# Kernel tuning notes

Hardware: AMD Instinct MI355X
Metric: run time of the kernel (lower is better)

The kernel has to match this reference:

```python
import jax, jax.numpy as jnp
import numpy as np

N_NODES = 32768
N_EDGES = 524288
NODE_DIM = 128
HIDDEN = 256
EDGE_DIM = 32


def setup_inputs() -> dict:
    key = jax.random.key(0)
    ks = jax.random.split(key, 12)
    s = 0.05
    return {
        "h": jax.random.normal(ks[0], (N_NODES, NODE_DIM), jnp.float32),
        "x": jax.random.normal(ks[1], (N_NODES, 3), jnp.float32) * 10.0,
        "edge_index": jax.random.randint(ks[2], (2, N_EDGES), 0, N_NODES, dtype=jnp.int32).astype(jnp.int64),
        "edge_dist": jax.random.uniform(ks[3], (N_EDGES,), jnp.float32) * 15.0,
        # edge_mlp: Linear(1, edge_dim) -> SiLU -> Linear(edge_dim, edge_dim)
        "We1": jax.random.normal(ks[4], (1, EDGE_DIM), jnp.float32) * s,
        "be1": jnp.zeros((EDGE_DIM,), jnp.float32),
        "We2": jax.random.normal(ks[5], (EDGE_DIM, EDGE_DIM), jnp.float32) * s,
        "be2": jnp.zeros((EDGE_DIM,), jnp.float32),
        # node_mlp: Linear(2*node+edge, hidden) -> SiLU -> Linear(hidden, node)
        "Wn1": jax.random.normal(ks[6], (2 * NODE_DIM + EDGE_DIM, HIDDEN), jnp.float32) * s,
        "bn1": jnp.zeros((HIDDEN,), jnp.float32),
        "Wn2": jax.random.normal(ks[7], (HIDDEN, NODE_DIM), jnp.float32) * s,
        "bn2": jnp.zeros((NODE_DIM,), jnp.float32),
        # coord_mlp: Linear(2*node+edge, hidden) -> SiLU -> Linear(hidden, 1, bias=False)
        "Wc1": jax.random.normal(ks[8], (2 * NODE_DIM + EDGE_DIM, HIDDEN), jnp.float32) * s,
        "bc1": jnp.zeros((HIDDEN,), jnp.float32),
        "Wc2": jax.random.normal(ks[9], (HIDDEN, 1), jnp.float32) * s,
    }


def reference(h, x, edge_index, edge_dist,
              We1, be1, We2, be2,
              Wn1, bn1, Wn2, bn2,
              Wc1, bc1, Wc2):
    src, dst = edge_index[0], edge_index[1]
    n_nodes = h.shape[0]

    # edge_mlp on scalar distances -> [E, edge_dim]
    edge_attr = jax.nn.silu(edge_dist[:, None] @ We1 + be1) @ We2 + be2

    # per-edge message input: [E, 2*node_dim + edge_dim]
    m_input = jnp.concatenate([h[src], h[dst], edge_attr], axis=-1)

    # node messages and scatter-add onto destination nodes
    m = jax.nn.silu(m_input @ Wn1 + bn1) @ Wn2 + bn2          # [E, node_dim]
    h_agg = jax.ops.segment_sum(m, dst, num_segments=n_nodes)  # [N, node_dim]

    # equivariant coordinate update along normalized edge direction
    coord_weight = jax.nn.silu(m_input @ Wc1 + bc1) @ Wc2      # [E, 1]
    dir_vec = x[src] - x[dst]                                  # [E, 3]
    dir_len = jnp.maximum(jnp.linalg.norm(dir_vec, axis=-1, keepdims=True), 1e-8)
    coord_update = coord_weight * (dir_vec / dir_len)          # [E, 3]
    x_agg = jax.ops.segment_sum(coord_update, dst, num_segments=n_nodes)

    return h + h_agg, x + x_agg
```

## Files before the change

kernel.cpp:

```cpp
#include <hip/hip_runtime.h>
#include <math.h>

#define N_NODES 32768
#define N_EDGES 524288
#define NODE_DIM 128
#define HIDDEN 256
#define EDGE_DIM 32
#define TE 64
#define NBLK (N_EDGES / TE)
#define ASTR 296
#define HSTR 264
#define MSTR 132

typedef __attribute__((ext_vector_type(8))) short bf16x8;
typedef __attribute__((ext_vector_type(16))) float f32x16;

__device__ __forceinline__ float silu_f(float v) {
    float e = __expf(-v);
    return v * __builtin_amdgcn_rcpf(1.0f + e);
}

__device__ __forceinline__ unsigned short f2bf_rne(float f) {
    union { float f; unsigned int u; } v; v.f = f;
    return (unsigned short)((v.u + 0x7fffu + ((v.u >> 16) & 1u)) >> 16);
}
__device__ __forceinline__ unsigned int pk_rne(float a, float b) {
    return (unsigned int)f2bf_rne(a) | ((unsigned int)f2bf_rne(b) << 16);
}
__device__ __forceinline__ unsigned int pkbf(float a, float b) {
    union { float f; unsigned int u; } ua, ub; ua.f = a; ub.f = b;
    return __builtin_amdgcn_perm(ub.u + 0x8000u, ua.u + 0x8000u, 0x07060302u);
}
__device__ __forceinline__ unsigned short f2bf_hu(float f) {
    union { float f; unsigned int u; } v; v.f = f;
    return (unsigned short)((v.u + 0x8000u) >> 16);
}

__device__ __forceinline__ int detect_is64(const void* ei, int t) {
    const unsigned int* ew = (const unsigned int*)ei;
    unsigned int hiw = ew[2 * (t & 63) + 1];
    return (__ballot(hiw != 0u) == 0ULL) ? 1 : 0;
}

#define WS_BIAS_OFF 1024
#define WS_W1S_OFF  69632
#define WS_W2S_OFF  364544
#define WS_CNT_OFF  430080
#define WS_CUR_OFF  561152
#define WS_PERM_OFF 692224
#define WS_PART_OFF 2789376
#define WS_HBF_OFF  2790400
#define WS_HBF_END  (WS_HBF_OFF + N_NODES * NODE_DIM * 2)

#define SEG_CNT  32768
#define SEG_W1S  147456
#define SEG_W2S  32768
#define SEG_BIAS 512
#define SEG_OUT  1073152
#define SEG_HBF  524288
#define PREP_TOT (SEG_CNT + SEG_W1S + SEG_W2S + SEG_BIAS + SEG_OUT + SEG_HBF)

__global__ void prep_all_kernel(const float* __restrict__ h, const float* __restrict__ x,
                                const float* __restrict__ We2, const float* __restrict__ be2,
                                const float* __restrict__ Wn1, const float* __restrict__ bn1,
                                const float* __restrict__ Wn2,
                                const float* __restrict__ Wc1, const float* __restrict__ bc1,
                                float* __restrict__ out, float* __restrict__ biasC,
                                unsigned short* __restrict__ W1s, unsigned short* __restrict__ W2s,
                                int* __restrict__ counts, unsigned short* __restrict__ hbf) {
    int i = blockIdx.x * 256 + threadIdx.x;
    if (i < SEG_CNT) { counts[i] = 0; return; }
    i -= SEG_CNT;
    if (i < SEG_W1S) {
        int jj = i & 7, ln = (i >> 3) & 63, rest = i >> 9;
        int step = rest % 18, tile = rest / 18;
        int n = tile * 32 + (ln & 31);
        int k = step * 16 + ((ln >> 5) * 8) + jj;
        float v;
        if (k < 256) {
            v = (n < 256) ? Wn1[k * 256 + n] : Wc1[k * 256 + (n - 256)];
        } else {
            int j = k - 256;
            float s = 0.0f;
            #pragma unroll 8
            for (int q = 0; q < 32; ++q)
                s += We2[j * 32 + q] * ((n < 256) ? Wn1[(256 + q) * 256 + n]
                                                  : Wc1[(256 + q) * 256 + (n - 256)]);
            v = s;
        }
        W1s[i] = f2bf_rne(v);
        return;
    }
    i -= SEG_W1S;
    if (i < SEG_W2S) {
        int jj = i & 7, ln = (i >> 3) & 63, rest = i >> 9;
        int step = rest & 15, tile = rest >> 4;
        int d = tile * 32 + (ln & 31);
        int k = step * 16 + ((ln >> 5) * 8) + jj;
        W2s[i] = f2bf_rne(Wn2[k * 128 + d]);
        return;
    }
    i -= SEG_W2S;
    if (i < SEG_BIAS) {
        int n = i;
        float s = (n < 256) ? bn1[n] : bc1[n - 256];
        #pragma unroll 8
        for (int q = 0; q < 32; ++q)
            s += be2[q] * ((n < 256) ? Wn1[(256 + q) * 256 + n]
                                     : Wc1[(256 + q) * 256 + (n - 256)]);
        biasC[n] = s;
        return;
    }
    i -= SEG_BIAS;
    if (i < SEG_OUT) {
        const int NH4 = N_NODES * NODE_DIM / 4;
        const float4* h4 = (const float4*)h;
        const float4* x4 = (const float4*)x;
        ((float4*)out)[i] = (i < NH4) ? h4[i] : x4[i - NH4];
        return;
    }
    i -= SEG_OUT;
    if (hbf != nullptr && i < SEG_HBF) {
        const float4* p = (const float4*)&h[i * 8];
        float4 v0 = p[0], v1 = p[1];
        uint4 o = make_uint4(pk_rne(v0.x, v0.y), pk_rne(v0.z, v0.w),
                             pk_rne(v1.x, v1.y), pk_rne(v1.z, v1.w));
        *(uint4*)&hbf[i * 8] = o;
    }
}

__global__ void hist_kernel(const void* __restrict__ ei, int* __restrict__ counts) {
    int is64 = detect_is64(ei, threadIdx.x);
    int e = blockIdx.x * 256 + threadIdx.x;
    int dst = is64 ? (int)((const long long*)ei)[N_EDGES + e]
                   : ((const int*)ei)[N_EDGES + e];
    atomicAdd(&counts[dst], 1);
}

__global__ __launch_bounds__(256)
void scanA_kernel(const int* __restrict__ counts, int* __restrict__ partials) {
    __shared__ int red[256];
    const int t = threadIdx.x;
    const int b = blockIdx.x;
    red[t] = counts[b * 256 + t];
    __syncthreads();
    #pragma unroll
    for (int s = 128; s > 0; s >>= 1) {
        if (t < s) red[t] += red[t + s];
        __syncthreads();
    }
    if (t == 0) partials[b] = red[0];
}

__global__ __launch_bounds__(256)
void scanC_kernel(const int* __restrict__ counts, const int* __restrict__ partials,
                  int* __restrict__ cursor) {
    __shared__ int pb[128];
    __shared__ int loc[256];
    const int t = threadIdx.x;
    const int b = blockIdx.x;
    if (t < 128) pb[t] = partials[t];
    int c = counts[b * 256 + t];
    loc[t] = c;
    __syncthreads();
    if (t == 0) {
        int s = 0;
        for (int j = 0; j < 128; ++j) { int v = pb[j]; pb[j] = s; s += v; }
    }
    #pragma unroll
    for (int d = 1; d < 256; d <<= 1) {
        int v = (t >= d) ? loc[t - d] : 0;
        __syncthreads();
        loc[t] += v;
        __syncthreads();
    }
    cursor[b * 256 + t] = pb[b] + loc[t] - c;
}

__global__ void place_kernel(const void* __restrict__ ei,
                             int* __restrict__ cursor, int* __restrict__ perm) {
    int is64 = detect_is64(ei, threadIdx.x);
    int e = blockIdx.x * 256 + threadIdx.x;
    int dst = is64 ? (int)((const long long*)ei)[N_EDGES + e]
                   : ((const int*)ei)[N_EDGES + e];
    int pos = atomicAdd(&cursor[dst], 1);
    perm[pos] = e;
}

__global__ __launch_bounds__(512, 4)
void egnn_mfma_kernel(const float* __restrict__ h, const float* __restrict__ x,
                      const void* __restrict__ ei, const float* __restrict__ dist,
                      const float* __restrict__ We1, const float* __restrict__ be1,
                      const float* __restrict__ bn2, const float* __restrict__ Wc2,
                      const float* __restrict__ biasC,
                      const unsigned short* __restrict__ W1s,
                      const unsigned short* __restrict__ W2s,
                      const int* __restrict__ perm,
                      const unsigned short* __restrict__ hbf,
                      float* __restrict__ out)
{
    __shared__ unsigned short smA[TE * ASTR];
    __shared__ int sidx[TE], didx[TE], eidx[TE];
    __shared__ float cw_s[TE];
    __shared__ float cxyz[3 * TE];

    unsigned short* smH = smA;
    float* smM = (float*)smA;

    const int t = threadIdx.x;
    const int lane = t & 63;
    const int wv = t >> 6;
    const int lo = lane & 31;
    const int hi = lane >> 5;
    const int swz = ((blockIdx.x & 7) * (NBLK / 8)) + (blockIdx.x >> 3);
    const int ebase = swz * TE;
    const int is64 = detect_is64(ei, t);

    if (t < 2 * TE) {
        int e = t & (TE - 1);
        int eid = perm[ebase + e];
        int which = t >> 6;
        long long pos = (long long)which * N_EDGES + eid;
        int idx = is64 ? (int)((const long long*)ei)[pos] : ((const int*)ei)[pos];
        if (which == 0) { sidx[e] = idx; eidx[e] = eid; }
        else didx[e] = idx;
        if (t < TE) cw_s[t] = 0.0f;
    }
    __syncthreads();

    if (hbf != nullptr) {
        #pragma unroll
        for (int it = 0; it < 4; ++it) {
            int id = it * 512 + t;
            int g = id & 15;
            int half = (id >> 4) & 1;
            int e = id >> 5;
            int node = half ? didx[e] : sidx[e];
            uint4 v = *(const uint4*)&hbf[node * NODE_DIM + 8 * g];
            *(uint4*)&smA[e * ASTR + half * NODE_DIM + 8 * g] = v;
        }
    } else {
        #pragma unroll
        for (int it = 0; it < 4; ++it) {
            int id = it * 512 + t;
            int g8 = id & 15;
            int half = (id >> 4) & 1;
            int e = id >> 5;
            int node = half ? didx[e] : sidx[e];
            const float4* p = (const float4*)&h[node * NODE_DIM + 8 * g8];
            float4 v0 = p[0], v1 = p[1];
            unsigned int a0 = pkbf(v0.x, v0.y), a1 = pkbf(v0.z, v0.w);
            unsigned int a2 = pkbf(v1.x, v1.y), a3 = pkbf(v1.z, v1.w);
            *(uint4*)&smA[e * ASTR + half * NODE_DIM + 8 * g8] = make_uint4(a0, a1, a2, a3);
        }
    }
    {
        int e = t >> 3;
        int j4 = (t & 7) * 4;
        float d = dist[eidx[e]];
        float s0 = silu_f(d * We1[j4 + 0] + be1[j4 + 0]);
        float s1 = silu_f(d * We1[j4 + 1] + be1[j4 + 1]);
        float s2 = silu_f(d * We1[j4 + 2] + be1[j4 + 2]);
        float s3 = silu_f(d * We1[j4 + 3] + be1[j4 + 3]);
        *(uint2*)&smA[e * ASTR + 2 * NODE_DIM + j4] = make_uint2(pkbf(s0, s1), pkbf(s2, s3));
    }
    if (t < TE) {
        int s = sidx[t], dn = didx[t];
        float dx = x[s * 3 + 0] - x[dn * 3 + 0];
        float dy = x[s * 3 + 1] - x[dn * 3 + 1];
        float dz = x[s * 3 + 2] - x[dn * 3 + 2];
        float len = fmaxf(sqrtf(dx * dx + dy * dy + dz * dz), 1e-8f);
        float inv = 1.0f / len;
        cxyz[t] = dx * inv; cxyz[TE + t] = dy * inv; cxyz[2 * TE + t] = dz * inv;
    }
    __syncthreads();

    f32x16 a00, a01, a10, a11;
    {
        int nb = wv * 64 + lo;
        float b0 = biasC[nb], b1 = biasC[nb + 32];
        #pragma unroll
        for (int r = 0; r < 16; ++r) { a00[r] = b0; a01[r] = b1; a10[r] = b0; a11[r] = b1; }
    }
    {
        const int aoff0 = lo * ASTR + hi * 8;
        const int aoff1 = (32 + lo) * ASTR + hi * 8;
        const int TS = 18 * 64 * 8;
        const int base = ((wv * 2 * 18) * 64 + lane) * 8;
        bf16x8 b0s[3], b1s[3];
        b0s[0] = *(const bf16x8*)&W1s[base];
        b1s[0] = *(const bf16x8*)&W1s[base + TS];
        b0s[1] = *(const bf16x8*)&W1s[base + 512];
        b1s[1] = *(const bf16x8*)&W1s[base + 512 + TS];
        #pragma unroll
        for (int step = 0; step < 18; ++step) {
            const int cur = step % 3;
            if (step + 2 < 18) {
                const int pf = (step + 2) % 3;
                b0s[pf] = *(const bf16x8*)&W1s[base + (step + 2) * 512];
                b1s[pf] = *(const bf16x8*)&W1s[base + (step + 2) * 512 + TS];
            }
            bf16x8 f0 = *(const bf16x8*)&smA[aoff0 + step * 16];
            bf16x8 f1 = *(const bf16x8*)&smA[aoff1 + step * 16];
            a00 = __builtin_amdgcn_mfma_f32_32x32x16_bf16(f0, b0s[cur], a00, 0, 0, 0);
            a10 = __builtin_amdgcn_mfma_f32_32x32x16_bf16(f1, b0s[cur], a10, 0, 0, 0);
            a01 = __builtin_amdgcn_mfma_f32_32x32x16_bf16(f0, b1s[cur], a01, 0, 0, 0);
            a11 = __builtin_amdgcn_mfma_f32_32x32x16_bf16(f1, b1s[cur], a11, 0, 0, 0);
        }
    }
    __syncthreads();

    const int rowbase = 4 * hi;
    if (wv < 4) {
        int jb = wv * 64 + lo;
        #pragma unroll
        for (int r = 0; r < 16; ++r) {
            int er = (r & 3) + 8 * (r >> 2) + rowbase;
            unsigned short* row0 = &smH[er * HSTR + jb];
            unsigned short* row1 = &smH[(er + 32) * HSTR + jb];
            row0[0]  = f2bf_hu(silu_f(a00[r]));
            row0[32] = f2bf_hu(silu_f(a01[r]));
            row1[0]  = f2bf_hu(silu_f(a10[r]));
            row1[32] = f2bf_hu(silu_f(a11[r]));
        }
    } else {
        int nc = (wv - 4) * 64 + lo;
        float w0 = Wc2[nc], w1 = Wc2[nc + 32];
        float p0[16], p1[16];
        #pragma unroll
        for (int r = 0; r < 16; ++r) {
            p0[r] = silu_f(a00[r]) * w0 + silu_f(a01[r]) * w1;
            p1[r] = silu_f(a10[r]) * w0 + silu_f(a11[r]) * w1;
        }
        #pragma unroll
        for (int off = 1; off < 32; off <<= 1) {
            #pragma unroll
            for (int r = 0; r < 16; ++r) {
                p0[r] += __shfl_xor(p0[r], off);
                p1[r] += __shfl_xor(p1[r], off);
            }
        }
        if (lo == 0) {
            #pragma unroll
            for (int r = 0; r < 16; ++r) {
                int er = (r & 3) + 8 * (r >> 2) + rowbase;
                atomicAdd(&cw_s[er], p0[r]);
                atomicAdd(&cw_s[er + 32], p1[r]);
            }
        }
    }
    __syncthreads();

    if (t < TE) {
        float w = cw_s[t];
        cxyz[t] *= w; cxyz[TE + t] *= w; cxyz[2 * TE + t] *= w;
    }

    {
        const int et = wv >> 2;
        const int dt = wv & 3;
        const int d = dt * 32 + lo;
        f32x16 acc;
        float bb = bn2[d];
        #pragma unroll
        for (int r = 0; r < 16; ++r) acc[r] = bb;
        const int hoff = (et * 32 + lo) * HSTR + hi * 8;
        const int wb = ((dt * 16) * 64 + lane) * 8;
        bf16x8 bs[3];
        bs[0] = *(const bf16x8*)&W2s[wb];
        bs[1] = *(const bf16x8*)&W2s[wb + 512];
        #pragma unroll
        for (int step = 0; step < 16; ++step) {
            const int cur = step % 3;
            if (step + 2 < 16) {
                const int pf = (step + 2) % 3;
                bs[pf] = *(const bf16x8*)&W2s[wb + (step + 2) * 512];
            }
            bf16x8 af = *(const bf16x8*)&smH[hoff + step * 16];
            acc = __builtin_amdgcn_mfma_f32_32x32x16_bf16(af, bs[cur], acc, 0, 0, 0);
        }
        __syncthreads();
        #pragma unroll
        for (int r = 0; r < 16; ++r) {
            int er = et * 32 + (r & 3) + 8 * (r >> 2) + rowbase;
            smM[er * MSTR + d] = acc[r];
        }
    }
    __syncthreads();

    {
        const int g = t >> 5;
        const int d4 = (t & 31) * 4;
        for (int e0 = g; e0 < TE; e0 += 16) {
            if (e0 > 0 && didx[e0] == didx[e0 - 1]) continue;
            float4 s = *(const float4*)&smM[e0 * MSTR + d4];
            int er = e0 + 1;
            while (er < TE && didx[er] == didx[e0]) {
                float4 v = *(const float4*)&smM[er * MSTR + d4];
                s.x += v.x; s.y += v.y; s.z += v.z; s.w += v.w;
                ++er;
            }
            float* dp = &out[didx[e0] * NODE_DIM + d4];
            if (e0 > 0 && er < TE) {
                float4 cur = *(const float4*)dp;
                cur.x += s.x; cur.y += s.y; cur.z += s.z; cur.w += s.w;
                *(float4*)dp = cur;
            } else {
                atomicAdd(dp + 0, s.x); atomicAdd(dp + 1, s.y);
                atomicAdd(dp + 2, s.z); atomicAdd(dp + 3, s.w);
            }
        }
    }
    if (t < TE) {
        int e0 = t;
        if (e0 == 0 || didx[e0] != didx[e0 - 1]) {
            float sx = cxyz[e0], sy = cxyz[TE + e0], sz = cxyz[2 * TE + e0];
            int er = e0 + 1;
            while (er < TE && didx[er] == didx[e0]) {
                sx += cxyz[er]; sy += cxyz[TE + er]; sz += cxyz[2 * TE + er];
                ++er;
            }
            float* xo = out + N_NODES * NODE_DIM + didx[e0] * 3;
            if (e0 > 0 && er < TE) {
                xo[0] += sx; xo[1] += sy; xo[2] += sz;
            } else {
                atomicAdd(xo + 0, sx); atomicAdd(xo + 1, sy); atomicAdd(xo + 2, sz);
            }
        }
    }
}

extern "C" void kernel_launch(void* const* d_in, const int* in_sizes, int n_in,
                              void* d_out, int out_size, void* d_ws, size_t ws_size,
                              hipStream_t stream) {
    const float* h    = (const float*)d_in[0];
    const float* x    = (const float*)d_in[1];
    const void*  ei   = d_in[2];
    const float* dist = (const float*)d_in[3];
    const float* We1  = (const float*)d_in[4];
    const float* be1  = (const float*)d_in[5];
    const float* We2  = (const float*)d_in[6];
    const float* be2  = (const float*)d_in[7];
    const float* Wn1  = (const float*)d_in[8];
    const float* bn1  = (const float*)d_in[9];
    const float* Wn2  = (const float*)d_in[10];
    const float* bn2  = (const float*)d_in[11];
    const float* Wc1  = (const float*)d_in[12];
    const float* bc1  = (const float*)d_in[13];
    const float* Wc2  = (const float*)d_in[14];
    float* out = (float*)d_out;

    float* biasC = (float*)((char*)d_ws + WS_BIAS_OFF);
    unsigned short* W1s = (unsigned short*)((char*)d_ws + WS_W1S_OFF);
    unsigned short* W2s = (unsigned short*)((char*)d_ws + WS_W2S_OFF);
    int* counts   = (int*)((char*)d_ws + WS_CNT_OFF);
    int* cursor   = (int*)((char*)d_ws + WS_CUR_OFF);
    int* perm     = (int*)((char*)d_ws + WS_PERM_OFF);
    int* partials = (int*)((char*)d_ws + WS_PART_OFF);
    unsigned short* hbf = (ws_size >= (size_t)WS_HBF_END)
                        ? (unsigned short*)((char*)d_ws + WS_HBF_OFF) : nullptr;

    prep_all_kernel<<<PREP_TOT / 256, 256, 0, stream>>>(
        h, x, We2, be2, Wn1, bn1, Wn2, Wc1, bc1,
        out, biasC, W1s, W2s, counts, hbf);

    hist_kernel<<<N_EDGES / 256, 256, 0, stream>>>(ei, counts);
    scanA_kernel<<<128, 256, 0, stream>>>(counts, partials);
    scanC_kernel<<<128, 256, 0, stream>>>(counts, partials, cursor);
    place_kernel<<<N_EDGES / 256, 256, 0, stream>>>(ei, cursor, perm);

    egnn_mfma_kernel<<<NBLK, 512, 0, stream>>>(
        h, x, ei, dist, We1, be1, bn2, Wc2, biasC, W1s, W2s, perm, hbf, out);
}
```

Measured before the change: 497.9 us.

## Halve edge tile to 32 with 256-thread blocks and remap MFMA work per wave

The per-block edge tile shrinks from 64 to 32 and the block size from 512 to 256 threads. Each wave now computes four 32-column hidden tiles (two for the node MLP, two for the coordinate MLP) over all 32 edges, and one 32-column output tile in the second GEMM, with double-buffered weight prefetch instead of triple-buffered. The goal is lower LDS and register use per block so more blocks fit per CU, giving more latency hiding. The cost is that every weight fetch from L2 now serves half as many edges, so total weight traffic doubles, and shorter per-block destination runs mean more boundary atomics in the scatter.

```diff
diff --git a/kernel.cpp b/kernel.cpp
--- a/kernel.cpp
+++ b/kernel.cpp
@@ -6,7 +6,7 @@
 #define NODE_DIM 128
 #define HIDDEN 256
 #define EDGE_DIM 32
-#define TE 64
+#define TE 32
 #define NBLK (N_EDGES / TE)
 #define ASTR 296
 #define HSTR 264
@@ -187,7 +187,7 @@
     perm[pos] = e;
 }
 
-__global__ __launch_bounds__(512, 4)
+__global__ __launch_bounds__(256, 4)
 void egnn_mfma_kernel(const float* __restrict__ h, const float* __restrict__ x,
                       const void* __restrict__ ei, const float* __restrict__ dist,
                       const float* __restrict__ We1, const float* __restrict__ be1,
@@ -219,7 +219,7 @@
     if (t < 2 * TE) {
         int e = t & (TE - 1);
         int eid = perm[ebase + e];
-        int which = t >> 6;
+        int which = t >> 5;
         long long pos = (long long)which * N_EDGES + eid;
         int idx = is64 ? (int)((const long long*)ei)[pos] : ((const int*)ei)[pos];
         if (which == 0) { sidx[e] = idx; eidx[e] = eid; }
@@ -231,7 +231,7 @@
     if (hbf != nullptr) {
         #pragma unroll
         for (int it = 0; it < 4; ++it) {
-            int id = it * 512 + t;
+            int id = it * 256 + t;
             int g = id & 15;
             int half = (id >> 4) & 1;
             int e = id >> 5;
@@ -242,7 +242,7 @@
     } else {
         #pragma unroll
         for (int it = 0; it < 4; ++it) {
-            int id = it * 512 + t;
+            int id = it * 256 + t;
             int g8 = id & 15;
             int half = (id >> 4) & 1;
             int e = id >> 5;
@@ -275,78 +275,70 @@
     }
     __syncthreads();
 
-    f32x16 a00, a01, a10, a11;
-    {
-        int nb = wv * 64 + lo;
-        float b0 = biasC[nb], b1 = biasC[nb + 32];
-        #pragma unroll
-        for (int r = 0; r < 16; ++r) { a00[r] = b0; a01[r] = b1; a10[r] = b0; a11[r] = b1; }
-    }
-    {
-        const int aoff0 = lo * ASTR + hi * 8;
-        const int aoff1 = (32 + lo) * ASTR + hi * 8;
+    f32x16 a0, a1, a2, a3;
+    {
+        float b0 = biasC[(wv     ) * 32 + lo];
+        float b1 = biasC[(wv +  4) * 32 + lo];
+        float b2 = biasC[(wv +  8) * 32 + lo];
+        float b3 = biasC[(wv + 12) * 32 + lo];
+        #pragma unroll
+        for (int r = 0; r < 16; ++r) { a0[r] = b0; a1[r] = b1; a2[r] = b2; a3[r] = b3; }
+    }
+    {
+        const int ao = lo * ASTR + hi * 8;
         const int TS = 18 * 64 * 8;
-        const int base = ((wv * 2 * 18) * 64 + lane) * 8;
-        bf16x8 b0s[3], b1s[3];
-        b0s[0] = *(const bf16x8*)&W1s[base];
-        b1s[0] = *(const bf16x8*)&W1s[base + TS];
-        b0s[1] = *(const bf16x8*)&W1s[base + 512];
-        b1s[1] = *(const bf16x8*)&W1s[base + 512 + TS];
+        const int b0 = (wv     ) * TS + lane * 8;
+        const int b1 = (wv +  4) * TS + lane * 8;
+        const int b2 = (wv +  8) * TS + lane * 8;
+        const int b3 = (wv + 12) * TS + lane * 8;
+        bf16x8 p0[2], p1[2], p2[2], p3[2];
+        p0[0] = *(const bf16x8*)&W1s[b0];
+        p1[0] = *(const bf16x8*)&W1s[b1];
+        p2[0] = *(const bf16x8*)&W1s[b2];
+        p3[0] = *(const bf16x8*)&W1s[b3];
         #pragma unroll
         for (int step = 0; step < 18; ++step) {
-            const int cur = step % 3;
-            if (step + 2 < 18) {
-                const int pf = (step + 2) % 3;
-                b0s[pf] = *(const bf16x8*)&W1s[base + (step + 2) * 512];
-                b1s[pf] = *(const bf16x8*)&W1s[base + (step + 2) * 512 + TS];
+            const int cur = step & 1, nxt = cur ^ 1;
+            if (step + 1 < 18) {
+                p0[nxt] = *(const bf16x8*)&W1s[b0 + (step + 1) * 512];
+                p1[nxt] = *(const bf16x8*)&W1s[b1 + (step + 1) * 512];
+                p2[nxt] = *(const bf16x8*)&W1s[b2 + (step + 1) * 512];
+                p3[nxt] = *(const bf16x8*)&W1s[b3 + (step + 1) * 512];
             }
-            bf16x8 f0 = *(const bf16x8*)&smA[aoff0 + step * 16];
-            bf16x8 f1 = *(const bf16x8*)&smA[aoff1 + step * 16];
-            a00 = __builtin_amdgcn_mfma_f32_32x32x16_bf16(f0, b0s[cur], a00, 0, 0, 0);
-            a10 = __builtin_amdgcn_mfma_f32_32x32x16_bf16(f1, b0s[cur], a10, 0, 0, 0);
-            a01 = __builtin_amdgcn_mfma_f32_32x32x16_bf16(f0, b1s[cur], a01, 0, 0, 0);
-            a11 = __builtin_amdgcn_mfma_f32_32x32x16_bf16(f1, b1s[cur], a11, 0, 0, 0);
+            bf16x8 f = *(const bf16x8*)&smA[ao + step * 16];
+            a0 = __builtin_amdgcn_mfma_f32_32x32x16_bf16(f, p0[cur], a0, 0, 0, 0);
+            a1 = __builtin_amdgcn_mfma_f32_32x32x16_bf16(f, p1[cur], a1, 0, 0, 0);
+            a2 = __builtin_amdgcn_mfma_f32_32x32x16_bf16(f, p2[cur], a2, 0, 0, 0);
+            a3 = __builtin_amdgcn_mfma_f32_32x32x16_bf16(f, p3[cur], a3, 0, 0, 0);
         }
     }
     __syncthreads();
 
     const int rowbase = 4 * hi;
-    if (wv < 4) {
-        int jb = wv * 64 + lo;
+    {
+        const int jb0 = (wv    ) * 32 + lo;
+        const int jb1 = (wv + 4) * 32 + lo;
         #pragma unroll
         for (int r = 0; r < 16; ++r) {
             int er = (r & 3) + 8 * (r >> 2) + rowbase;
-            unsigned short* row0 = &smH[er * HSTR + jb];
-            unsigned short* row1 = &smH[(er + 32) * HSTR + jb];
-            row0[0]  = f2bf_hu(silu_f(a00[r]));
-            row0[32] = f2bf_hu(silu_f(a01[r]));
-            row1[0]  = f2bf_hu(silu_f(a10[r]));
-            row1[32] = f2bf_hu(silu_f(a11[r]));
-        }
-    } else {
-        int nc = (wv - 4) * 64 + lo;
-        float w0 = Wc2[nc], w1 = Wc2[nc + 32];
-        float p0[16], p1[16];
-        #pragma unroll
-        for (int r = 0; r < 16; ++r) {
-            p0[r] = silu_f(a00[r]) * w0 + silu_f(a01[r]) * w1;
-            p1[r] = silu_f(a10[r]) * w0 + silu_f(a11[r]) * w1;
-        }
+            smH[er * HSTR + jb0] = f2bf_hu(silu_f(a0[r]));
+            smH[er * HSTR + jb1] = f2bf_hu(silu_f(a1[r]));
+        }
+        float w2 = Wc2[(wv    ) * 32 + lo];
+        float w3 = Wc2[(wv + 4) * 32 + lo];
+        float p[16];
+        #pragma unroll
+        for (int r = 0; r < 16; ++r)
+            p[r] = silu_f(a2[r]) * w2 + silu_f(a3[r]) * w3;
         #pragma unroll
         for (int off = 1; off < 32; off <<= 1) {
             #pragma unroll
-            for (int r = 0; r < 16; ++r) {
-                p0[r] += __shfl_xor(p0[r], off);
-                p1[r] += __shfl_xor(p1[r], off);
-            }
+            for (int r = 0; r < 16; ++r) p[r] += __shfl_xor(p[r], off);
         }
         if (lo == 0) {
             #pragma unroll
-            for (int r = 0; r < 16; ++r) {
-                int er = (r & 3) + 8 * (r >> 2) + rowbase;
-                atomicAdd(&cw_s[er], p0[r]);
-                atomicAdd(&cw_s[er + 32], p1[r]);
-            }
+            for (int r = 0; r < 16; ++r)
+                atomicAdd(&cw_s[(r & 3) + 8 * (r >> 2) + rowbase], p[r]);
         }
     }
     __syncthreads();
@@ -357,32 +349,27 @@
     }
 
     {
-        const int et = wv >> 2;
-        const int dt = wv & 3;
-        const int d = dt * 32 + lo;
+        const int d = wv * 32 + lo;
         f32x16 acc;
         float bb = bn2[d];
         #pragma unroll
         for (int r = 0; r < 16; ++r) acc[r] = bb;
-        const int hoff = (et * 32 + lo) * HSTR + hi * 8;
-        const int wb = ((dt * 16) * 64 + lane) * 8;
-        bf16x8 bs[3];
+        const int hoff = lo * HSTR + hi * 8;
+        const int wb = wv * (16 * 64 * 8) + lane * 8;
+        bf16x8 bs[2];
         bs[0] = *(const bf16x8*)&W2s[wb];
-        bs[1] = *(const bf16x8*)&W2s[wb + 512];
         #pragma unroll
         for (int step = 0; step < 16; ++step) {
-            const int cur = step % 3;
-            if (step + 2 < 16) {
-                const int pf = (step + 2) % 3;
-                bs[pf] = *(const bf16x8*)&W2s[wb + (step + 2) * 512];
-            }
+            const int cur = step & 1, nxt = cur ^ 1;
+            if (step + 1 < 16)
+                bs[nxt] = *(const bf16x8*)&W2s[wb + (step + 1) * 512];
             bf16x8 af = *(const bf16x8*)&smH[hoff + step * 16];
             acc = __builtin_amdgcn_mfma_f32_32x32x16_bf16(af, bs[cur], acc, 0, 0, 0);
         }
         __syncthreads();
         #pragma unroll
         for (int r = 0; r < 16; ++r) {
-            int er = et * 32 + (r & 3) + 8 * (r >> 2) + rowbase;
+            int er = (r & 3) + 8 * (r >> 2) + rowbase;
             smM[er * MSTR + d] = acc[r];
         }
     }
@@ -391,7 +378,7 @@
     {
         const int g = t >> 5;
         const int d4 = (t & 31) * 4;
-        for (int e0 = g; e0 < TE; e0 += 16) {
+        for (int e0 = g; e0 < TE; e0 += 8) {
             if (e0 > 0 && didx[e0] == didx[e0 - 1]) continue;
             float4 s = *(const float4*)&smM[e0 * MSTR + d4];
             int er = e0 + 1;
@@ -469,6 +456,6 @@
     scanC_kernel<<<128, 256, 0, stream>>>(counts, partials, cursor);
     place_kernel<<<N_EDGES / 256, 256, 0, stream>>>(ei, cursor, perm);
 
-    egnn_mfma_kernel<<<NBLK, 512, 0, stream>>>(
+    egnn_mfma_kernel<<<NBLK, 256, 0, stream>>>(
         h, x, ei, dist, We1, be1, bn2, Wc2, biasC, W1s, W2s, perm, hbf, out);
 }
```

Result: faster. 472.8 us (-5.0%).
